# Kernel optimization log

Measured on AMD Instinct MI355X. Metric: run time of the kernel, lower is better.

Reference implementation:

```python
import jax, jax.numpy as jnp
import numpy as np

WS = 7            # cubic window
HEADS = 6
DIM = 96          # attention channel dim (concat of two half-streams)
CH = 48           # per-stream channels (dim // 2)
HID = 384         # int(dim * mlp_ratio)
N = WS ** 3       # 343 tokens per window
EPS = 1e-5


def _rel_pos_index():
    c = np.stack(np.meshgrid(np.arange(WS), np.arange(WS), np.arange(WS), indexing='ij')).reshape(3, -1)
    rel = (c[:, :, None] - c[:, None, :]).transpose(1, 2, 0) + (WS - 1)
    rel[:, :, 0] *= (2 * WS - 1) * (2 * WS - 1)
    rel[:, :, 1] *= (2 * WS - 1)
    return rel.sum(-1)  # (N, N) int

RPI = jnp.asarray(_rel_pos_index())


def _ln(x, g, b):
    m = x.mean(-1, keepdims=True)
    v = ((x - m) ** 2).mean(-1, keepdims=True)
    return (x - m) * jax.lax.rsqrt(v + EPS) * g + b


def _win_part(x):
    B, H, W, T, C = x.shape
    x = x.reshape(B, H // WS, WS, W // WS, WS, T // WS, WS, C)
    return x.transpose(0, 1, 3, 5, 2, 4, 6, 7).reshape(-1, WS, WS, WS, C)


def _win_rev(w, B, H, W, T):
    C = w.shape[-1]
    x = w.reshape(B, H // WS, W // WS, T // WS, WS, WS, WS, C)
    return x.transpose(0, 1, 4, 2, 5, 3, 6, 7).reshape(B, H, W, T, C)


def _chessboard(wa, wb, gd, gh, gw):
    C = wa.shape[-1]
    a = wa.reshape(gd, gh, gw, WS, WS, WS, C)
    b = wb.reshape(gd, gh, gw, WS, WS, WS, C)
    i = jnp.arange(gd)[:, None, None]
    j = jnp.arange(gh)[None, :, None]
    k = jnp.arange(gw)[None, None, :]
    m = (((i + j + k) % 2) == 0)[..., None, None, None, None]
    return (jnp.where(m, a, b).reshape(-1, WS, WS, WS, C),
            jnp.where(m, b, a).reshape(-1, WS, WS, WS, C))


def _attn(x, mask, rpb, qkv_w, qkv_b, proj_w, proj_b):
    B_, n, C = x.shape
    hd = C // HEADS
    qkv = (x @ qkv_w + qkv_b).reshape(B_, n, 3, HEADS, hd).transpose(2, 0, 3, 1, 4)
    q, k, v = qkv[0] * (hd ** -0.5), qkv[1], qkv[2]
    att = jnp.einsum('bhnd,bhmd->bhnm', q, k)
    att = att + rpb[RPI].transpose(2, 0, 1)[None]   # relative position bias gather
    att = att + mask[:, None]                        # shift mask; B_ == nW since B == 1
    att = jax.nn.softmax(att, axis=-1)
    out = jnp.einsum('bhnm,bhmd->bhnd', att, v).transpose(0, 2, 1, 3).reshape(B_, n, C)
    return out @ proj_w + proj_b


def _mlp(x, w1, b1, w2, b2):
    return jax.nn.gelu(x @ w1 + b1, approximate=False) @ w2 + b2


def _forward(x_a, x_b, mask_matrix, n1a_g, n1a_b, n1b_g, n1b_b,
             rpb_a, qkvw_a, qkvb_a, projw_a, projb_a,
             rpb_b, qkvw_b, qkvb_b, projw_b, projb_b,
             n2a_g, n2a_b, n2b_g, n2b_b,
             fc1w_a, fc1b_a, fc2w_a, fc2b_a, fc1w_b, fc1b_b, fc2w_b, fc2b_b,
             gw1, gw2, gb2, H, W, T):
    B, L, _ = x_a.shape
    sa0, sb0 = x_a, x_b
    a = _ln(x_a, n1a_g, n1a_b).reshape(B, H, W, T, CH)
    b = _ln(x_b, n1b_g, n1b_b).reshape(B, H, W, T, CH)
    # chessboard cross-stream shuffle of windows (shifted-window branch)
    ca, cb = _chessboard(_win_part(a), _win_part(b), H // WS, W // WS, T // WS)
    a_cr = _win_rev(ca, B, H, W, T)
    b_cr = _win_rev(cb, B, H, W, T)
    neg, pos, dims = (-3, -3, -3), (3, 3, 3), (1, 2, 3)
    sa, sb = jnp.roll(a, neg, dims), jnp.roll(b, neg, dims)
    sac, sbc = jnp.roll(a_cr, neg, dims), jnp.roll(b_cr, neg, dims)
    xa_w = _win_part(jnp.concatenate([sa, sbc], -1)).reshape(-1, N, DIM)
    xb_w = _win_part(jnp.concatenate([sb, sac], -1)).reshape(-1, N, DIM)
    oa = _attn(xa_w, mask_matrix, rpb_a, qkvw_a, qkvb_a, projw_a, projb_a)
    ob = _attn(xb_w, mask_matrix, rpb_b, qkvw_b, qkvb_b, projw_b, projb_b)
    oa = jnp.roll(_win_rev(oa.reshape(-1, WS, WS, WS, DIM), B, H, W, T), pos, dims)[..., :CH].reshape(B, L, CH)
    ob = jnp.roll(_win_rev(ob.reshape(-1, WS, WS, WS, DIM), B, H, W, T), pos, dims)[..., :CH].reshape(B, L, CH)
    x_a = sa0 + oa
    x_b = sb0 + ob
    x_a = x_a + _mlp(_ln(x_a, n2a_g, n2a_b), fc1w_a, fc1b_a, fc2w_a, fc2b_a)
    x_b = x_b + _mlp(_ln(x_b, n2b_g, n2b_b), fc1w_b, fc1b_b, fc2w_b, fc2b_b)
    g = jax.nn.sigmoid(jnp.maximum(x_a.mean(1) @ gw1, 0.0) @ gw2 + gb2)[:, :, None]  # (B,1,1)
    x_a = x_a + g * x_b
    return x_a, x_b


def setup_inputs():
    key = jax.random.key(0)
    ks = iter(jax.random.split(key, 24))
    H = W = T = 35
    L = H * W * T
    nW = (H // WS) * (W // WS) * (T // WS)
    p = lambda shape: jax.random.normal(next(ks), shape, jnp.float32) * 0.02
    d = {
        'x_a': jax.random.normal(next(ks), (1, L, CH), jnp.float32),
        'x_b': jax.random.normal(next(ks), (1, L, CH), jnp.float32),
        'mask_matrix': jax.random.normal(next(ks), (nW, N, N), jnp.float32),
        'n1a_g': jnp.ones((CH,), jnp.float32), 'n1a_b': jnp.zeros((CH,), jnp.float32),
        'n1b_g': jnp.ones((CH,), jnp.float32), 'n1b_b': jnp.zeros((CH,), jnp.float32),
        'rpb_a': p(((2 * WS - 1) ** 3, HEADS)),
        'qkvw_a': p((DIM, 3 * DIM)), 'qkvb_a': jnp.zeros((3 * DIM,), jnp.float32),
        'projw_a': p((DIM, DIM)), 'projb_a': jnp.zeros((DIM,), jnp.float32),
        'rpb_b': p(((2 * WS - 1) ** 3, HEADS)),
        'qkvw_b': p((DIM, 3 * DIM)), 'qkvb_b': jnp.zeros((3 * DIM,), jnp.float32),
        'projw_b': p((DIM, DIM)), 'projb_b': jnp.zeros((DIM,), jnp.float32),
        'n2a_g': jnp.ones((CH,), jnp.float32), 'n2a_b': jnp.zeros((CH,), jnp.float32),
        'n2b_g': jnp.ones((CH,), jnp.float32), 'n2b_b': jnp.zeros((CH,), jnp.float32),
        'fc1w_a': p((CH, HID)), 'fc1b_a': jnp.zeros((HID,), jnp.float32),
        'fc2w_a': p((HID, CH)), 'fc2b_a': jnp.zeros((CH,), jnp.float32),
        'fc1w_b': p((CH, HID)), 'fc1b_b': jnp.zeros((HID,), jnp.float32),
        'fc2w_b': p((HID, CH)), 'fc2b_b': jnp.zeros((CH,), jnp.float32),
        'gw1': p((CH, CH // 4)), 'gw2': p((CH // 4, 1)),
        'gb2': jnp.full((1,), -2.0, jnp.float32),
        'H': H, 'W': W, 'T': T,
    }
    return d


def reference(x_a, x_b, mask_matrix, n1a_g, n1a_b, n1b_g, n1b_b,
              rpb_a, qkvw_a, qkvb_a, projw_a, projb_a,
              rpb_b, qkvw_b, qkvb_b, projw_b, projb_b,
              n2a_g, n2a_b, n2b_g, n2b_b,
              fc1w_a, fc1b_a, fc2w_a, fc2b_a, fc1w_b, fc1b_b, fc2w_b, fc2b_b,
              gw1, gw2, gb2, H, W, T):
    return _forward(x_a, x_b, mask_matrix, n1a_g, n1a_b, n1b_g, n1b_b,
                    rpb_a, qkvw_a, qkvb_a, projw_a, projb_a,
                    rpb_b, qkvw_b, qkvb_b, projw_b, projb_b,
                    n2a_g, n2a_b, n2b_g, n2b_b,
                    fc1w_a, fc1b_a, fc2w_a, fc2b_a, fc1w_b, fc1b_b, fc2w_b, fc2b_b,
                    gw1, gw2, gb2, H, W, T)
```

## Files before the change

kernel.cpp:

```cpp
#include <hip/hip_runtime.h>
#include <hip/hip_fp16.h>

#define LQ    42875
#define NTOK  343
#define X1SZ  2058000

#define OFF_MEAN 0
#define OFF_QKV  36928
#define OFF_WF   12500000
#define OFF_RPB  12600000
#define OFF_MASKH 13400000
#define QKV_BYTES_NEEDED 56100000ull
#define MASKH_BYTES_NEEDED 83100000ull

typedef _Float16 f16x8 __attribute__((ext_vector_type(8)));
typedef float f32x4 __attribute__((ext_vector_type(4)));
union B128 { uint4 u; f16x8 h; _Float16 e[8]; };
union U2H { unsigned u; __half2 h; };

__device__ __forceinline__ int src_index(int w, int i, int& par) {
  int gi = w / 25, gj = (w / 5) % 5, gk = w % 5;
  int ph = i / 49, pw = (i / 7) % 7, pt = i % 7;
  int hs = gi * 7 + ph + 3; if (hs >= 35) hs -= 35;
  int wd = gj * 7 + pw + 3; if (wd >= 35) wd -= 35;
  int td = gk * 7 + pt + 3; if (td >= 35) td -= 35;
  par = ((hs / 7) + (wd / 7) + (td / 7)) & 1;
  return (hs * 35 + wd) * 35 + td;
}

__global__ __launch_bounds__(256) void k_pack(
    const float* __restrict__ w1a, const float* __restrict__ w1b,
    const float* __restrict__ w2a, const float* __restrict__ w2b,
    const float* __restrict__ qwa, const float* __restrict__ qwb,
    float* __restrict__ ws) {
  if (blockIdx.x == 0 && threadIdx.x < 49) ws[OFF_MEAN + threadIdx.x] = 0.f;
  int idx = blockIdx.x * 256 + threadIdx.x;
  if (idx >= 17664) return;
  uint4* WFB = (uint4*)(ws + OFF_WF);
  unsigned short h[8];
  uint4* dst;
  if (idx < 10752) {
    int s = idx / 5376, r = idx - s * 5376;
    uint4* WF = WFB + (size_t)s * 5376;
    if (r < 3072) {
      int jn = r / 128, t = r - jn * 128, kk = t / 64, lane = t - kk * 64;
      int q = lane >> 4, n = lane & 15;
      const float* w1 = s ? w1b : w1a;
      int j = jn * 16 + n;
#pragma unroll
      for (int e = 0; e < 8; e++) {
        int k = kk * 32 + q * 8 + e;
        float v = (k < 48) ? w1[k * 384 + j] : 0.f;
        h[e] = __half_as_ushort(__float2half(v));
      }
    } else {
      int rr = r - 3072;
      int kt = rr / 192, t = rr - kt * 192, cn = t / 64, lane = t - cn * 64;
      int q = lane >> 4, n = lane & 15;
      const float* w2 = s ? w2b : w2a;
      int c = cn * 16 + n;
#pragma unroll
      for (int e = 0; e < 8; e++) {
        int j = kt * 32 + q * 8 + e;
        h[e] = __half_as_ushort(__float2half(w2[j * 48 + c]));
      }
    }
    dst = WF + r;
  } else {
    int idx2 = idx - 10752;
    int s = idx2 / 3456, r = idx2 - s * 3456;
    int jn = r / 192, t = r - jn * 192, kk = t / 64, lane = t - kk * 64;
    int q = lane >> 4, n = lane & 15;
    const float* qw = s ? qwb : qwa;
    int j = jn * 16 + n;
#pragma unroll
    for (int e = 0; e < 8; e++) {
      int k = kk * 32 + q * 8 + e;
      h[e] = __half_as_ushort(__float2half(qw[k * 288 + j]));
    }
    dst = WFB + 10752 + (size_t)s * 3456 + r;
  }
  uint4 u;
  u.x = (unsigned)h[0] | ((unsigned)h[1] << 16);
  u.y = (unsigned)h[2] | ((unsigned)h[3] << 16);
  u.z = (unsigned)h[4] | ((unsigned)h[5] << 16);
  u.w = (unsigned)h[6] | ((unsigned)h[7] << 16);
  *dst = u;
}

__global__ __launch_bounds__(256) void k_rpb(
    const float* __restrict__ rpa, const float* __restrict__ rpbp,
    float* __restrict__ ws) {
  int sh = blockIdx.y;
  int s = sh / 6, h = sh - s * 6;
  int idx = blockIdx.x * 256 + threadIdx.x;
  if (idx >= 117649) return;
  int ir = idx / 343, j = idx - ir * 343;
  int bi = (ir / 49) * 169 + ((ir / 7) % 7) * 13 + (ir % 7) + 1098;
  int bj = (j / 49) * 169 + ((j / 7) % 7) * 13 + (j % 7);
  const float* rp = s ? rpbp : rpa;
  ((__half*)(ws + OFF_RPB))[(size_t)sh * 117992 + ir * 344 + j] =
      __float2half(rp[(bi - bj) * 6 + h]);
}

__global__ __launch_bounds__(256) void k_maskh(
    const float* __restrict__ mask, __half* __restrict__ mh) {
  int idx = blockIdx.x * 256 + threadIdx.x;
  if (idx >= 42875 * 86) return;
  int row = idx / 86, c = (idx - row * 86) * 4;
  const float* src = mask + (size_t)row * 343 + c;
  float v0 = src[0];
  float v1 = (c + 1 < 343) ? src[1] : 0.f;
  float v2 = (c + 2 < 343) ? src[2] : 0.f;
  float v3 = (c + 3 < 343) ? src[3] : 0.f;
  U2H a, b;
  a.h = __floats2half2_rn(v0, v1);
  b.h = __floats2half2_rn(v2, v3);
  uint2 o; o.x = a.u; o.y = b.u;
  *(uint2*)(mh + (size_t)row * 344 + c) = o;
}

__global__ __launch_bounds__(256) void k_qkv(
    const float* __restrict__ xa, const float* __restrict__ xb,
    const float* __restrict__ ga, const float* __restrict__ ba,
    const float* __restrict__ gb, const float* __restrict__ bb,
    const float* __restrict__ qba, const float* __restrict__ qbb,
    const float* __restrict__ ws, __half* __restrict__ qkvh) {
  __shared__ uint4 LDSB[2368];
  int s = blockIdx.z;
  int tid = threadIdx.x;
  int wid = tid >> 6, lane = tid & 63;
  int quad = lane >> 4, n15 = lane & 15;
  uint4* WR = LDSB + wid * 592;
  _Float16* th = (_Float16*)WR;
  int tbase = blockIdx.x * 64 + wid * 16;

  if (lane < 32) {
    int tt = lane & 15, which = lane >> 4;
    int t = tbase + tt;
    float v[48];
    bool wr = false, dup = false;
    if (t < LQ) {
      int w = t / 343, i = t - w * 343;
      int par; int src = src_index(w, i, par);
      const float* xr; const float* G; const float* B;
      bool doit;
      if (which == 0) { xr = (s ? xb : xa) + src * 48; G = s ? gb : ga; B = s ? bb : ba; doit = true; dup = (par == 1); }
      else            { xr = (s ? xa : xb) + src * 48; G = s ? ga : gb; B = s ? ba : bb; doit = (par == 0); }
      if (doit) {
        float sm = 0.f, sq = 0.f;
#pragma unroll
        for (int q4 = 0; q4 < 12; q4++) {
          float4 tv = ((const float4*)xr)[q4];
          v[4 * q4] = tv.x; v[4 * q4 + 1] = tv.y; v[4 * q4 + 2] = tv.z; v[4 * q4 + 3] = tv.w;
          sm += tv.x + tv.y + tv.z + tv.w;
          sq += tv.x * tv.x + tv.y * tv.y + tv.z * tv.z + tv.w * tv.w;
        }
        float m = sm * (1.f / 48.f);
        float r = rsqrtf(sq * (1.f / 48.f) - m * m + 1e-5f);
#pragma unroll
        for (int k = 0; k < 48; k++) v[k] = (v[k] - m) * r * G[k] + B[k];
        wr = true;
      }
    } else if (which == 0) {
#pragma unroll
      for (int k = 0; k < 48; k++) v[k] = 0.f;
      wr = true; dup = true;
    }
    if (wr) {
#pragma unroll
      for (int c6 = 0; c6 < 6; c6++) {
        unsigned short h[8];
#pragma unroll
        for (int e = 0; e < 8; e++) h[e] = __half_as_ushort(__float2half(v[c6 * 8 + e]));
        uint4 u;
        u.x = (unsigned)h[0] | ((unsigned)h[1] << 16);
        u.y = (unsigned)h[2] | ((unsigned)h[3] << 16);
        u.z = (unsigned)h[4] | ((unsigned)h[5] << 16);
        u.w = (unsigned)h[6] | ((unsigned)h[7] << 16);
        WR[(which * 6 + c6) * 16 + tt] = u;
        if (dup) WR[(6 + c6) * 16 + tt] = u;
      }
    }
  }

  B128 ax0, ax1, ax2;
  ax0.u = WR[(0 + quad) * 16 + n15];
  ax1.u = WR[(4 + quad) * 16 + n15];
  ax2.u = WR[(8 + quad) * 16 + n15];

  const uint4* QF = (const uint4*)(ws + OFF_WF) + 10752 + (size_t)s * 3456;
  const float* QB = s ? qbb : qba;
  const f32x4 ZC = {0.f, 0.f, 0.f, 0.f};

  for (int jn = 0; jn < 18; jn++) {
    B128 b0, b1, b2;
    b0.u = QF[(jn * 3 + 0) * 64 + lane];
    b1.u = QF[(jn * 3 + 1) * 64 + lane];
    b2.u = QF[(jn * 3 + 2) * 64 + lane];
    f32x4 c = __builtin_amdgcn_mfma_f32_16x16x32_f16(ax0.h, b0.h, ZC, 0, 0, 0);
    c = __builtin_amdgcn_mfma_f32_16x16x32_f16(ax1.h, b1.h, c, 0, 0, 0);
    c = __builtin_amdgcn_mfma_f32_16x16x32_f16(ax2.h, b2.h, c, 0, 0, 0);
    float bias = QB[jn * 16 + n15];
    float scale = (jn < 6) ? 0.25f : 1.0f;
#pragma unroll
    for (int r = 0; r < 4; r++)
      th[(quad * 4 + r) * 296 + jn * 16 + n15] = (_Float16)((c[r] + bias) * scale);
  }
  for (int e = lane; e < 576; e += 64) {
    int row = e / 36, cc = e - row * 36;
    int t = tbase + row;
    if (t < LQ)
      ((uint4*)qkvh)[(size_t)(s * LQ + t) * 36 + cc] = WR[row * 37 + cc];
  }
}

template <bool H16>
__global__ __launch_bounds__(256) void k_attn(
    const __half* __restrict__ rpbmat,
    const void* __restrict__ maskp, __half* __restrict__ qkvh) {
  int bid = blockIdx.x;
  int xcd = bid & 7, q8 = bid >> 3;
  int u = q8 / 12, inst = q8 - u * 12;
  int w = u * 8 + xcd;
  if (w >= 125) return;
  int s = inst & 1, h = inst >> 1;

  __shared__ uint4 FRAG[1408];
  uint4* Kf4 = FRAG;
  uint4* Vf4 = FRAG + 704;
  _Float16* Vfh = (_Float16*)(FRAG + 704);

  int tid = threadIdx.x;
  const uint4 Z4 = {0u, 0u, 0u, 0u};
  for (int e = tid; e < 1408; e += 256) FRAG[e] = Z4;
  __syncthreads();

  size_t wbase = (size_t)((s * 125 + w) * NTOK) * 288;
  for (int i = tid; i < NTOK; i += 256) {
    const uint4* row = (const uint4*)(qkvh + wbase + (size_t)i * 288) + (h * 2);
    uint4 k0 = row[12], k1 = row[13];
    B128 v0, v1; v0.u = row[24]; v1.u = row[25];
    int n = i & 15, it = i >> 4;
    Kf4[it * 32 + n] = k0;
    Kf4[it * 32 + 16 + n] = k1;
    int il = i & 31, t5 = i >> 5;
    int qq, ee;
    if (il < 16) { qq = il >> 2; ee = il & 3; }
    else { qq = (il - 16) >> 2; ee = 4 + ((il - 16) & 3); }
    int vb = (t5 * 64 + qq * 16) * 8 + ee;
#pragma unroll
    for (int d = 0; d < 8; d++) {
      Vfh[vb + d * 8] = v0.e[d];
      Vfh[vb + (d + 8) * 8] = v1.e[d];
    }
  }
  __syncthreads();

  int wid = tid >> 6, lane = tid & 63;
  int quad = lane >> 4, n15 = lane & 15;
  const f32x4 ZC = {0.f, 0.f, 0.f, 0.f};
  __half* obh = qkvh;
  const __half* rbase = rpbmat + (size_t)(s * 6 + h) * 117992;
  int ja0 = quad * 4;

  for (int it = wid; it < 22; it += 4) {
    int i0 = it * 16;
    int irow = i0 + n15; if (irow > 342) irow = 342;
    const __half* rrow = rbase + (size_t)irow * 344;
    const __half* mrow = nullptr; const float* mrowf = nullptr;
    if constexpr (H16) mrow = (const __half*)maskp + ((size_t)w * 343 + irow) * 344;
    else mrowf = (const float*)maskp + ((size_t)w * 343 + irow) * 343;

    B128 qbits;
    int qtok = i0 + n15;
    if (quad < 2 && qtok < NTOK)
      qbits.u = *((const uint4*)(qkvh + wbase + (size_t)qtok * 288) + h * 2 + (quad & 1));
    else
      qbits.u = Z4;
    f32x4 acc = ZC;
    float ls = 0.f;

    float bcur[8], bnxt[8];
    auto loadb = [&](int jt, float* b) {
      if constexpr (H16) {
        const __half* mp = mrow + jt * 32 + ja0;
        const __half* rp2 = rrow + jt * 32 + ja0;
        uint2 ma = *(const uint2*)mp;
        uint2 mb = *(const uint2*)(mp + 16);
        uint2 ra = *(const uint2*)rp2;
        uint2 rb = *(const uint2*)(rp2 + 16);
        U2H x0, x1, x2, x3, y0, y1, y2, y3;
        x0.u = ma.x; x1.u = ma.y; x2.u = mb.x; x3.u = mb.y;
        y0.u = ra.x; y1.u = ra.y; y2.u = rb.x; y3.u = rb.y;
        float2 f;
        f = __half22float2(__hadd2(x0.h, y0.h)); b[0] = f.x; b[1] = f.y;
        f = __half22float2(__hadd2(x1.h, y1.h)); b[2] = f.x; b[3] = f.y;
        f = __half22float2(__hadd2(x2.h, y2.h)); b[4] = f.x; b[5] = f.y;
        f = __half22float2(__hadd2(x3.h, y3.h)); b[6] = f.x; b[7] = f.y;
      } else {
        const float* mp = mrowf + jt * 32 + ja0;
        const __half* rp2 = rrow + jt * 32 + ja0;
#pragma unroll
        for (int r = 0; r < 4; r++) {
          b[r] = mp[r] + __half2float(rp2[r]);
          b[4 + r] = mp[16 + r] + __half2float(rp2[16 + r]);
        }
      }
    };
    loadb(0, bcur);

    for (int j32 = 0; j32 < 11; j32++) {
      if (j32 < 10) loadb(j32 + 1, bnxt);
      B128 kb0, kb1;
      kb0.u = Kf4[(j32 * 2) * 32 + ((quad & 1) << 4) + n15];
      kb1.u = Kf4[(j32 * 2 + 1) * 32 + ((quad & 1) << 4) + n15];
      if (quad >= 2) { kb0.u = Z4; kb1.u = Z4; }
      f32x4 s0 = __builtin_amdgcn_mfma_f32_16x16x32_f16(kb0.h, qbits.h, ZC, 0, 0, 0);
      f32x4 s1 = __builtin_amdgcn_mfma_f32_16x16x32_f16(kb1.h, qbits.h, ZC, 0, 0, 0);
      bool last = (j32 == 10);
      float p0[4], p1[4];
#pragma unroll
      for (int r = 0; r < 4; r++) {
        float b1 = bcur[4 + r];
        if (last && (quad * 4 + r) >= 7) b1 = -1e30f;
        p0[r] = __expf(s0[r] + bcur[r]);
        p1[r] = __expf(s1[r] + b1);
        ls += p0[r] + p1[r];
      }
      U2H c0, c1, c2, c3;
      c0.h = __floats2half2_rn(p0[0], p0[1]);
      c1.h = __floats2half2_rn(p0[2], p0[3]);
      c2.h = __floats2half2_rn(p1[0], p1[1]);
      c3.h = __floats2half2_rn(p1[2], p1[3]);
      B128 pa;
      pa.u.x = c0.u; pa.u.y = c1.u; pa.u.z = c2.u; pa.u.w = c3.u;
      B128 vbits; vbits.u = Vf4[j32 * 64 + lane];
      acc = __builtin_amdgcn_mfma_f32_16x16x32_f16(pa.h, vbits.h, acc, 0, 0, 0);
#pragma unroll
      for (int e = 0; e < 8; e++) bcur[e] = bnxt[e];
    }
    ls += __shfl_xor(ls, 16);
    ls += __shfl_xor(ls, 32);
#pragma unroll
    for (int r = 0; r < 4; r++) {
      float lr = __shfl(ls, quad * 4 + r);
      int ir = i0 + quad * 4 + r;
      if (ir < 343)
        obh[wbase + (size_t)ir * 288 + h * 16 + n15] = __float2half(acc[r] * (1.f / lr));
    }
  }
}

__global__ __launch_bounds__(384) void k_proj(
    const __half* __restrict__ qkvh,
    const float* __restrict__ xa0, const float* __restrict__ xb0,
    const float* __restrict__ pwa, const float* __restrict__ pba,
    const float* __restrict__ pwb, const float* __restrict__ pbb,
    float* __restrict__ out) {
  int sw = blockIdx.x; int s = sw / 125, w = sw - s * 125;
  int i = threadIdx.x;
  if (i >= NTOK) return;
  const float* Wt = s ? pwb : pwa;
  const float* Bi = s ? pbb : pba;
  const uint4* orow = (const uint4*)(qkvh + (size_t)((s * 125 + w) * NTOK + i) * 288);
  float acc[48];
#pragma unroll
  for (int c = 0; c < 48; c++) acc[c] = 0.f;
#pragma unroll
  for (int k8 = 0; k8 < 12; k8++) {
    B128 ov; ov.u = orow[k8];
#pragma unroll
    for (int e = 0; e < 8; e++) {
      float x = (float)ov.e[e];
      const float* wr = Wt + (k8 * 8 + e) * 96;
#pragma unroll
      for (int c = 0; c < 48; c++) acc[c] = fmaf(x, wr[c], acc[c]);
    }
  }
  int par; int src = src_index(w, i, par);
  const float* x0 = (s ? xb0 : xa0) + src * 48;
  float* dst = out + s * X1SZ + src * 48;
#pragma unroll
  for (int q = 0; q < 12; q++) {
    float4 xv = ((const float4*)x0)[q];
    float4 o;
    o.x = xv.x + acc[4 * q + 0] + Bi[4 * q + 0];
    o.y = xv.y + acc[4 * q + 1] + Bi[4 * q + 1];
    o.z = xv.z + acc[4 * q + 2] + Bi[4 * q + 2];
    o.w = xv.w + acc[4 * q + 3] + Bi[4 * q + 3];
    ((float4*)dst)[q] = o;
  }
}

__global__ __launch_bounds__(256) void k_mlp(
    const float* __restrict__ g2a, const float* __restrict__ b2a,
    const float* __restrict__ g2b, const float* __restrict__ b2b,
    const float* __restrict__ fb1a, const float* __restrict__ fb2a,
    const float* __restrict__ fb1b, const float* __restrict__ fb2b,
    float* __restrict__ out, float* __restrict__ ws) {
  __shared__ uint4 Xf[512];
  __shared__ uint4 tbu[320];
  __shared__ float red[48];
  int s = blockIdx.z;
  int tid = threadIdx.x;
  int wid = tid >> 6, lane = tid & 63;
  int quad = lane >> 4, n15 = lane & 15;
  if (tid < 48) red[tid] = 0.f;
  __syncthreads();

  const float* B1 = s ? fb1b : fb1a;
  const float* B2 = s ? fb2b : fb2a;
  const uint4* W1F = (const uint4*)(ws + OFF_WF) + (size_t)s * 5376;
  const uint4* W2F = W1F + 3072;
  int tbase = blockIdx.x * 64 + wid * 16;
  float* outs = out + (size_t)s * X1SZ;

  if (lane < 16) {
    int t = tbase + lane;
    float v[48];
    if (t < LQ) {
      const float* row = outs + (size_t)t * 48;
      float sm = 0.f, sq = 0.f;
#pragma unroll
      for (int q4 = 0; q4 < 12; q4++) {
        float4 tv = ((const float4*)row)[q4];
        v[4 * q4] = tv.x; v[4 * q4 + 1] = tv.y; v[4 * q4 + 2] = tv.z; v[4 * q4 + 3] = tv.w;
        sm += tv.x + tv.y + tv.z + tv.w;
        sq += tv.x * tv.x + tv.y * tv.y + tv.z * tv.z + tv.w * tv.w;
      }
      float m = sm * (1.f / 48.f);
      float r = rsqrtf(sq * (1.f / 48.f) - m * m + 1e-5f);
      const float* G = s ? g2b : g2a;
      const float* B = s ? b2b : b2a;
#pragma unroll
      for (int k = 0; k < 48; k++) v[k] = (v[k] - m) * r * G[k] + B[k];
    } else {
#pragma unroll
      for (int k = 0; k < 48; k++) v[k] = 0.f;
    }
#pragma unroll
    for (int kc = 0; kc < 8; kc++) {
      uint4 u = {0u, 0u, 0u, 0u};
      if (kc < 6) {
        unsigned short h[8];
#pragma unroll
        for (int e = 0; e < 8; e++) h[e] = __half_as_ushort(__float2half(v[kc * 8 + e]));
        u.x = (unsigned)h[0] | ((unsigned)h[1] << 16);
        u.y = (unsigned)h[2] | ((unsigned)h[3] << 16);
        u.z = (unsigned)h[4] | ((unsigned)h[5] << 16);
        u.w = (unsigned)h[6] | ((unsigned)h[7] << 16);
      }
      Xf[wid * 128 + kc * 16 + lane] = u;
    }
  }

  _Float16* mytb = (_Float16*)(tbu + wid * 80);
  const uint4* mytb4 = tbu + wid * 80;
  const f32x4 ZC = {0.f, 0.f, 0.f, 0.f};
  f32x4 oacc[3] = {ZC, ZC, ZC};
  B128 ax0, ax1;
  ax0.u = Xf[wid * 128 + quad * 16 + n15];
  ax1.u = Xf[wid * 128 + (4 + quad) * 16 + n15];

  for (int kt = 0; kt < 12; kt++) {
    int jn0 = kt * 2, jn1 = jn0 + 1;
    B128 w0, w1, w2, w3;
    w0.u = W1F[jn0 * 128 + lane];
    w1.u = W1F[jn0 * 128 + 64 + lane];
    w2.u = W1F[jn1 * 128 + lane];
    w3.u = W1F[jn1 * 128 + 64 + lane];
    f32x4 a0 = __builtin_amdgcn_mfma_f32_16x16x32_f16(ax0.h, w0.h, ZC, 0, 0, 0);
    a0 = __builtin_amdgcn_mfma_f32_16x16x32_f16(ax1.h, w1.h, a0, 0, 0, 0);
    f32x4 a1 = __builtin_amdgcn_mfma_f32_16x16x32_f16(ax0.h, w2.h, ZC, 0, 0, 0);
    a1 = __builtin_amdgcn_mfma_f32_16x16x32_f16(ax1.h, w3.h, a1, 0, 0, 0);
    float bz0 = B1[jn0 * 16 + n15], bz1 = B1[jn1 * 16 + n15];
#pragma unroll
    for (int r = 0; r < 4; r++) {
      float h0 = a0[r] + bz0;
      h0 = 0.5f * h0 * (1.f + erff(h0 * 0.70710678118654752f));
      float h1 = a1[r] + bz1;
      h1 = 0.5f * h1 * (1.f + erff(h1 * 0.70710678118654752f));
      int rowb = (quad * 4 + r) * 40;
      mytb[rowb + n15] = (_Float16)h0;
      mytb[rowb + 16 + n15] = (_Float16)h1;
    }
    B128 pa; pa.u = mytb4[n15 * 5 + quad];
    B128 c0, c1, c2;
    c0.u = W2F[kt * 192 + lane];
    c1.u = W2F[kt * 192 + 64 + lane];
    c2.u = W2F[kt * 192 + 128 + lane];
    oacc[0] = __builtin_amdgcn_mfma_f32_16x16x32_f16(pa.h, c0.h, oacc[0], 0, 0, 0);
    oacc[1] = __builtin_amdgcn_mfma_f32_16x16x32_f16(pa.h, c1.h, oacc[1], 0, 0, 0);
    oacc[2] = __builtin_amdgcn_mfma_f32_16x16x32_f16(pa.h, c2.h, oacc[2], 0, 0, 0);
  }

  float b2v[3];
#pragma unroll
  for (int cn = 0; cn < 3; cn++) b2v[cn] = B2[cn * 16 + n15];
  float gsum[3] = {0.f, 0.f, 0.f};
#pragma unroll
  for (int r = 0; r < 4; r++) {
    int t = tbase + quad * 4 + r;
    bool val = t < LQ;
    float* orow = outs + (size_t)(val ? t : 0) * 48;
#pragma unroll
    for (int cn = 0; cn < 3; cn++) {
      float fin = 0.f;
      if (val) {
        fin = orow[cn * 16 + n15] + oacc[cn][r] + b2v[cn];
        orow[cn * 16 + n15] = fin;
      }
      gsum[cn] += fin;
    }
  }
  if (s == 0) {
#pragma unroll
    for (int cn = 0; cn < 3; cn++) {
      float v = gsum[cn];
      v += __shfl_xor(v, 16); v += __shfl_xor(v, 32);
      if (quad == 0) atomicAdd(&red[cn * 16 + n15], v);
    }
  }
  __syncthreads();
  if (s == 0 && tid < 48) atomicAdd(ws + OFF_MEAN + tid, red[tid]);
}

__global__ __launch_bounds__(256) void k_gadd(
    float* __restrict__ out, const float* __restrict__ ws_mean,
    const float* __restrict__ gw1, const float* __restrict__ gw2,
    const float* __restrict__ gb2) {
  __shared__ float gs;
  int tid = threadIdx.x;
  if (tid < 64) {
    float t = 0.f;
    if (tid < 12) {
      for (int c = 0; c < 48; c++)
        t = fmaf(ws_mean[c] * (1.f / (float)LQ), gw1[c * 12 + tid], t);
      t = fmaxf(t, 0.f) * gw2[tid];
    }
    for (int off = 32; off > 0; off >>= 1) t += __shfl_down(t, off);
    if (tid == 0) gs = 1.f / (1.f + __expf(-(t + gb2[0])));
  }
  __syncthreads();
  float gv = gs;
  int i = blockIdx.x * 256 + tid;
  if (i >= X1SZ / 4) return;
  float4* a = (float4*)out;
  const float4* b = (const float4*)(out + X1SZ);
  float4 x = a[i], y = b[i];
  x.x = fmaf(gv, y.x, x.x);
  x.y = fmaf(gv, y.y, x.y);
  x.z = fmaf(gv, y.z, x.z);
  x.w = fmaf(gv, y.w, x.w);
  a[i] = x;
}

extern "C" void kernel_launch(void* const* d_in, const int* in_sizes, int n_in,
                              void* d_out, int out_size, void* d_ws, size_t ws_size,
                              hipStream_t stream) {
  const float* xa    = (const float*)d_in[0];
  const float* xb    = (const float*)d_in[1];
  const float* mask  = (const float*)d_in[2];
  const float* n1ag  = (const float*)d_in[3];
  const float* n1ab  = (const float*)d_in[4];
  const float* n1bg  = (const float*)d_in[5];
  const float* n1bb  = (const float*)d_in[6];
  const float* rpba  = (const float*)d_in[7];
  const float* qkvwa = (const float*)d_in[8];
  const float* qkvba = (const float*)d_in[9];
  const float* pwa   = (const float*)d_in[10];
  const float* pba   = (const float*)d_in[11];
  const float* rpbb  = (const float*)d_in[12];
  const float* qkvwb = (const float*)d_in[13];
  const float* qkvbb = (const float*)d_in[14];
  const float* pwb   = (const float*)d_in[15];
  const float* pbb   = (const float*)d_in[16];
  const float* n2ag  = (const float*)d_in[17];
  const float* n2ab  = (const float*)d_in[18];
  const float* n2bg  = (const float*)d_in[19];
  const float* n2bb  = (const float*)d_in[20];
  const float* w1a   = (const float*)d_in[21];
  const float* fb1a  = (const float*)d_in[22];
  const float* w2a   = (const float*)d_in[23];
  const float* fb2a  = (const float*)d_in[24];
  const float* w1b   = (const float*)d_in[25];
  const float* fb1b  = (const float*)d_in[26];
  const float* w2b   = (const float*)d_in[27];
  const float* fb2b  = (const float*)d_in[28];
  const float* gw1   = (const float*)d_in[29];
  const float* gw2   = (const float*)d_in[30];
  const float* gb2   = (const float*)d_in[31];
  float* ws  = (float*)d_ws;
  float* out = (float*)d_out;

  if (ws_size < QKV_BYTES_NEEDED) return;
  __half* qkvh = (__half*)(ws + OFF_QKV);
  bool bigmask = ws_size >= MASKH_BYTES_NEEDED;

  hipLaunchKernelGGL(k_pack, dim3(69), dim3(256), 0, stream,
                     w1a, w1b, w2a, w2b, qkvwa, qkvwb, ws);
  hipLaunchKernelGGL(k_rpb, dim3(460, 12), dim3(256), 0, stream,
                     rpba, rpbb, ws);
  if (bigmask)
    hipLaunchKernelGGL(k_maskh, dim3(14405), dim3(256), 0, stream,
                       mask, (__half*)(ws + OFF_MASKH));
  hipLaunchKernelGGL(k_qkv, dim3(670, 1, 2), dim3(256), 0, stream,
                     xa, xb, n1ag, n1ab, n1bg, n1bb,
                     qkvba, qkvbb, ws, qkvh);
  if (bigmask)
    hipLaunchKernelGGL((k_attn<true>), dim3(1536), dim3(256), 0, stream,
                       (const __half*)(ws + OFF_RPB),
                       (const void*)(ws + OFF_MASKH), qkvh);
  else
    hipLaunchKernelGGL((k_attn<false>), dim3(1536), dim3(256), 0, stream,
                       (const __half*)(ws + OFF_RPB), (const void*)mask, qkvh);
  hipLaunchKernelGGL(k_proj, dim3(250), dim3(384), 0, stream,
                     qkvh, xa, xb, pwa, pba, pwb, pbb, out);
  hipLaunchKernelGGL(k_mlp, dim3(670, 1, 2), dim3(256), 0, stream,
                     n2ag, n2ab, n2bg, n2bb,
                     fb1a, fb2a, fb1b, fb2b, out, ws);
  hipLaunchKernelGGL(k_gadd, dim3(2011), dim3(256), 0, stream,
                     out, ws + OFF_MEAN, gw1, gw2, gb2);
}
```

Baseline: 423.8 us.

## Compute output projection with fp16 MFMA using prepacked projection weights

The projection kernel used a scalar per-thread FP32 FMA loop over 96 inputs and 48 outputs, launched as 250 blocks of 384 threads. It now packs the projection weights to fp16 MFMA fragment layout in k_pack and computes each 16-token tile with three chained 16x16x32 f16 MFMAs per output group, across 1340 blocks. This removes a large scalar FMA workload and raises parallelism. In exchange the weights are rounded to fp16, and the residual stores are now scalar and scattered rather than float4.

Result: faster. 376.0 us (-11.3%).

```diff
diff --git a/kernel.cpp b/kernel.cpp
--- a/kernel.cpp
+++ b/kernel.cpp
@@ -32,10 +32,11 @@
     const float* __restrict__ w1a, const float* __restrict__ w1b,
     const float* __restrict__ w2a, const float* __restrict__ w2b,
     const float* __restrict__ qwa, const float* __restrict__ qwb,
+    const float* __restrict__ pwa, const float* __restrict__ pwb,
     float* __restrict__ ws) {
   if (blockIdx.x == 0 && threadIdx.x < 49) ws[OFF_MEAN + threadIdx.x] = 0.f;
   int idx = blockIdx.x * 256 + threadIdx.x;
-  if (idx >= 17664) return;
+  if (idx >= 18816) return;
   uint4* WFB = (uint4*)(ws + OFF_WF);
   unsigned short h[8];
   uint4* dst;
@@ -66,7 +67,7 @@
       }
     }
     dst = WF + r;
-  } else {
+  } else if (idx < 17664) {
     int idx2 = idx - 10752;
     int s = idx2 / 3456, r = idx2 - s * 3456;
     int jn = r / 192, t = r - jn * 192, kk = t / 64, lane = t - kk * 64;
@@ -79,6 +80,19 @@
       h[e] = __half_as_ushort(__float2half(qw[k * 288 + j]));
     }
     dst = WFB + 10752 + (size_t)s * 3456 + r;
+  } else {
+    int idx3 = idx - 17664;
+    int s = idx3 / 576, r = idx3 - s * 576;
+    int jn = r / 192, t = r - jn * 192, kk = t / 64, lane = t - kk * 64;
+    int q = lane >> 4, n = lane & 15;
+    const float* pw = s ? pwb : pwa;
+    int c = jn * 16 + n;
+#pragma unroll
+    for (int e = 0; e < 8; e++) {
+      int k = kk * 32 + q * 8 + e;
+      h[e] = __half_as_ushort(__float2half(pw[k * 96 + c]));
+    }
+    dst = WFB + 17664 + (size_t)s * 576 + r;
   }
   uint4 u;
   u.x = (unsigned)h[0] | ((unsigned)h[1] << 16);
@@ -352,44 +366,55 @@
   }
 }
 
-__global__ __launch_bounds__(384) void k_proj(
+__global__ __launch_bounds__(256) void k_proj(
     const __half* __restrict__ qkvh,
     const float* __restrict__ xa0, const float* __restrict__ xb0,
-    const float* __restrict__ pwa, const float* __restrict__ pba,
-    const float* __restrict__ pwb, const float* __restrict__ pbb,
-    float* __restrict__ out) {
-  int sw = blockIdx.x; int s = sw / 125, w = sw - s * 125;
-  int i = threadIdx.x;
-  if (i >= NTOK) return;
-  const float* Wt = s ? pwb : pwa;
+    const float* __restrict__ pba, const float* __restrict__ pbb,
+    const float* __restrict__ ws, float* __restrict__ out) {
+  int s = blockIdx.z;
+  int tid = threadIdx.x;
+  int wid = tid >> 6, lane = tid & 63;
+  int quad = lane >> 4, n15 = lane & 15;
+  int t0 = blockIdx.x * 64 + wid * 16;
+
+  int tA = t0 + n15; if (tA >= LQ) tA = LQ - 1;
+  const uint4* orow = (const uint4*)qkvh + (size_t)(s * LQ + tA) * 36;
+  B128 a0, a1, a2;
+  a0.u = orow[quad];
+  a1.u = orow[4 + quad];
+  a2.u = orow[8 + quad];
+
+  const uint4* PF = (const uint4*)(ws + OFF_WF) + 17664 + (size_t)s * 576;
   const float* Bi = s ? pbb : pba;
-  const uint4* orow = (const uint4*)(qkvh + (size_t)((s * 125 + w) * NTOK + i) * 288);
-  float acc[48];
-#pragma unroll
-  for (int c = 0; c < 48; c++) acc[c] = 0.f;
-#pragma unroll
-  for (int k8 = 0; k8 < 12; k8++) {
-    B128 ov; ov.u = orow[k8];
-#pragma unroll
-    for (int e = 0; e < 8; e++) {
-      float x = (float)ov.e[e];
-      const float* wr = Wt + (k8 * 8 + e) * 96;
-#pragma unroll
-      for (int c = 0; c < 48; c++) acc[c] = fmaf(x, wr[c], acc[c]);
-    }
-  }
-  int par; int src = src_index(w, i, par);
-  const float* x0 = (s ? xb0 : xa0) + src * 48;
-  float* dst = out + s * X1SZ + src * 48;
-#pragma unroll
-  for (int q = 0; q < 12; q++) {
-    float4 xv = ((const float4*)x0)[q];
-    float4 o;
-    o.x = xv.x + acc[4 * q + 0] + Bi[4 * q + 0];
-    o.y = xv.y + acc[4 * q + 1] + Bi[4 * q + 1];
-    o.z = xv.z + acc[4 * q + 2] + Bi[4 * q + 2];
-    o.w = xv.w + acc[4 * q + 3] + Bi[4 * q + 3];
-    ((float4*)dst)[q] = o;
+  const f32x4 ZC = {0.f, 0.f, 0.f, 0.f};
+  f32x4 c[3];
+#pragma unroll
+  for (int jn = 0; jn < 3; jn++) {
+    B128 b0, b1, b2;
+    b0.u = PF[(jn * 3 + 0) * 64 + lane];
+    b1.u = PF[(jn * 3 + 1) * 64 + lane];
+    b2.u = PF[(jn * 3 + 2) * 64 + lane];
+    f32x4 cc = __builtin_amdgcn_mfma_f32_16x16x32_f16(a0.h, b0.h, ZC, 0, 0, 0);
+    cc = __builtin_amdgcn_mfma_f32_16x16x32_f16(a1.h, b1.h, cc, 0, 0, 0);
+    cc = __builtin_amdgcn_mfma_f32_16x16x32_f16(a2.h, b2.h, cc, 0, 0, 0);
+    c[jn] = cc;
+  }
+  float bias[3];
+#pragma unroll
+  for (int jn = 0; jn < 3; jn++) bias[jn] = Bi[jn * 16 + n15];
+#pragma unroll
+  for (int r = 0; r < 4; r++) {
+    int t = t0 + quad * 4 + r;
+    if (t >= LQ) continue;
+    int w = t / 343, i = t - w * 343;
+    int par; int src = src_index(w, i, par);
+    const float* x0 = (s ? xb0 : xa0) + (size_t)src * 48;
+    float* dst = out + (size_t)s * X1SZ + (size_t)src * 48;
+#pragma unroll
+    for (int jn = 0; jn < 3; jn++) {
+      int col = jn * 16 + n15;
+      dst[col] = x0[col] + c[jn][r] + bias[jn];
+    }
   }
 }
 
@@ -598,8 +623,8 @@
   __half* qkvh = (__half*)(ws + OFF_QKV);
   bool bigmask = ws_size >= MASKH_BYTES_NEEDED;
 
-  hipLaunchKernelGGL(k_pack, dim3(69), dim3(256), 0, stream,
-                     w1a, w1b, w2a, w2b, qkvwa, qkvwb, ws);
+  hipLaunchKernelGGL(k_pack, dim3(74), dim3(256), 0, stream,
+                     w1a, w1b, w2a, w2b, qkvwa, qkvwb, pwa, pwb, ws);
   hipLaunchKernelGGL(k_rpb, dim3(460, 12), dim3(256), 0, stream,
                      rpba, rpbb, ws);
   if (bigmask)
@@ -615,8 +640,8 @@
   else
     hipLaunchKernelGGL((k_attn<false>), dim3(1536), dim3(256), 0, stream,
                        (const __half*)(ws + OFF_RPB), (const void*)mask, qkvh);
-  hipLaunchKernelGGL(k_proj, dim3(250), dim3(384), 0, stream,
-                     qkvh, xa, xb, pwa, pba, pwb, pbb, out);
+  hipLaunchKernelGGL(k_proj, dim3(670, 1, 2), dim3(256), 0, stream,
+                     qkvh, xa, xb, pba, pbb, ws, out);
   hipLaunchKernelGGL(k_mlp, dim3(670, 1, 2), dim3(256), 0, stream,
                      n2ag, n2ab, n2bg, n2bb,
                      fb1a, fb2a, fb1b, fb2b, out, ws);
```
